# Performance work log

Hardware: AMD Instinct MI355X
Metric: run time of the kernel (lower is better)

Reference implementation:

```python
import jax, jax.numpy as jnp
import numpy as np

# dims: S sets, M max items, DIN input feat, DM model dim (= head_size), H heads, L layers
S, M, DIN, DM, H, DH, L = 48, 128, 128, 128, 4, 128, 2
ALPHA = 0.3  # tf.keras.layers.LeakyReLU default alpha


def gelu(x):
    return jax.nn.gelu(x, approximate=False)  # tf.nn.gelu default is exact


def leaky(x):
    return jnp.where(x >= 0, x, ALPHA * x)


def set_norm(x, size):
    # masked per-set normalization over all items*features; pad rows (feature-sum == 0) are zeroed
    d = x.shape[-1]
    mask = (jnp.sum(x, axis=-1, keepdims=True) != 0).astype(x.dtype)  # [S,M,1]
    denom = size * d  # [S]
    mean = jnp.sum(x, axis=(1, 2)) / denom
    diff = x - mean[:, None, None]
    var = jnp.sum(jnp.square(diff) * mask, axis=(1, 2)) / denom
    return diff / (jnp.sqrt(var)[:, None, None] + 1e-8) * mask


def masked_softmax(s):
    # original masks by *nonzero score values*, not an additive bias
    mask = s != 0
    e = jnp.where(mask, jnp.exp(s - jnp.max(s, axis=-1, keepdims=True)), 0.0)
    return e / (jnp.sum(e, axis=-1, keepdims=True) + 1e-10)


def attention(x, wq, wk, wv, wh):
    split = lambda z: z.reshape(z.shape[0], z.shape[1], H, DH).transpose(0, 2, 1, 3)  # [S,H,M,D]
    q, k, v = split(x @ wq), split(x @ wk), split(x @ wv)
    s = jnp.einsum('shmd,shnd->shmn', q, k) / np.float32(np.sqrt(DH))
    a = masked_softmax(s)
    o = jnp.einsum('shmn,shnd->shmd', a, v).transpose(0, 2, 1, 3).reshape(x.shape[0], x.shape[1], H * DH)
    return o @ wh


def forward(x, size, W_proj, Wq, Wk, Wv, Wh, Wfc, Wc, w2):
    mask = (jnp.sum(x != 0, axis=-1, keepdims=True) > 0).astype(x.dtype)  # [S,M,1] valid-item mask
    h = gelu(x @ W_proj) * mask
    for l in range(L):
        a = attention(h, Wq[l], Wk[l], Wv[l], Wh[l]) * mask
        h = set_norm(h + a, size)
        f = gelu(h @ Wfc[l]) * mask
        h = set_norm(h + f, size)
    # cross_set_score (tuple branch, x == y): pairwise per-head set scores
    z = (h @ Wc).reshape(h.shape[0], h.shape[1], H, DH).transpose(0, 2, 1, 3)  # [S,H,M,D]
    s = leaky(jnp.einsum('jhmd,ihnd->jihmn', z, z) / np.float32(np.sqrt(DH)))  # [Sy,Sx,H,My,Mx]
    scores = jnp.sum(s, axis=(-1, -2)) / size[None, :, None] / np.float32(M)  # [Sy,Sx,H]
    return scores @ w2  # [Sy,Sx,1]


def setup_inputs() -> dict:
    key = jax.random.key(0)
    ks = jax.random.split(key, 10)
    x = jax.random.normal(ks[0], (S, M, DIN), jnp.float32)
    x_size = jax.random.randint(ks[1], (S,), 1, M + 1, jnp.int32)
    x = x * (jnp.arange(M)[None, :] < x_size[:, None])[:, :, None]  # zero-pad beyond set size
    sc = lambda n: np.float32(1.0 / np.sqrt(n))
    W_proj = jax.random.normal(ks[2], (DIN, DM), jnp.float32) * sc(DIN)
    Wq = jax.random.normal(ks[3], (L, DM, H * DH), jnp.float32) * sc(DM)
    Wk = jax.random.normal(ks[4], (L, DM, H * DH), jnp.float32) * sc(DM)
    Wv = jax.random.normal(ks[5], (L, DM, H * DH), jnp.float32) * sc(DM)
    Wh = jax.random.normal(ks[6], (L, H * DH, DM), jnp.float32) * sc(H * DH)
    Wfc = jax.random.normal(ks[7], (L, DM, DM), jnp.float32) * sc(DM)
    Wc = jax.random.normal(ks[8], (DM, H * DH), jnp.float32) * sc(DM)
    w2 = jax.random.normal(ks[9], (H, 1), jnp.float32) * sc(H)
    return dict(x=x, x_size=x_size, W_proj=W_proj, Wq=Wq, Wk=Wk, Wv=Wv, Wh=Wh, Wfc=Wfc, Wc=Wc, w2=w2)


def reference(x, x_size, W_proj, Wq, Wk, Wv, Wh, Wfc, Wc, w2):
    size = jnp.maximum(x_size, 1).astype(jnp.float32)
    return forward(x, size, W_proj, Wq, Wk, Wv, Wh, Wfc, Wc, w2)
```

## Files before the change

kernel.cpp:

```cpp
#include <hip/hip_runtime.h>
#include <hip/hip_bf16.h>
#include <math.h>

typedef unsigned short u16;
typedef short bf16x8 __attribute__((ext_vector_type(8)));
typedef float f32x4 __attribute__((ext_vector_type(4)));
typedef float f32x16 __attribute__((ext_vector_type(16)));

__device__ __forceinline__ u16 f2b(float f){
  union { float f; unsigned u; } c; c.f = f;
  unsigned u = c.u;
  unsigned r = (u + 0x7fffu + ((u >> 16) & 1u)) >> 16;
  return (u16)r;
}
__device__ __forceinline__ unsigned pack2(float a, float b){
  return (unsigned)f2b(a) | ((unsigned)f2b(b) << 16);
}
__device__ __forceinline__ float gelu_f(float x){
  return 0.5f * x * (1.0f + erff(x * 0.70710678118654752f));
}

__global__ __launch_bounds__(256) void prep_weights(
    const float* __restrict__ Wproj, const float* __restrict__ Wq,
    const float* __restrict__ Wk,    const float* __restrict__ Wv,
    const float* __restrict__ Whp,   const float* __restrict__ Wfc,
    const float* __restrict__ Wc,    u16* __restrict__ wT)
{
  __shared__ __align__(16) u16 Ah[128*136];
  __shared__ __align__(16) u16 Bv[128*136];
  int bid = blockIdx.x, tid = threadIdx.x;
  if (bid < 312) {
    int cid = bid * 256 + tid;
    if (cid >= 34816 && cid < 67584) return;
    int region, lh = 0, c;
    if      (cid < 2048)  { region = 0; c = cid; }
    else if (cid < 18432) { int o = cid - 2048;  region = 1; lh = o >> 11; c = o & 2047; }
    else if (cid < 34816) { int o = cid - 18432; region = 2; lh = o >> 11; c = o & 2047; }
    else if (cid < 71680) { int o = cid - 67584; region = 5; lh = o >> 11; c = o & 2047; }
    else                  { int o = cid - 71680; region = 6; lh = o >> 11; c = o & 2047; }
    int l16 = c & 15, quad = (c >> 4) & 3, ks = (c >> 6) & 3, nt = c >> 8;
    int n = nt * 16 + l16, kb = ks * 32 + quad * 8;
    int l = lh >> 2, hh = lh & 3;
    const float rs = 0.08838834764831845f;
    u16 tmp[8];
#pragma unroll
    for (int e = 0; e < 8; ++e) {
      int k = kb + e;
      float v;
      switch (region) {
        case 0: v = Wproj[k * 128 + n]; break;
        case 1: v = Wq[l * 65536 + k * 512 + hh * 128 + n] * rs; break;
        case 2: v = Wk[l * 65536 + k * 512 + hh * 128 + n]; break;
        case 5: v = Wfc[lh * 16384 + k * 128 + n]; break;
        default: v = Wc[k * 512 + lh * 128 + n]; break;
      }
      tmp[e] = f2b(v);
    }
    *(uint4*)(wT + (size_t)cid * 8) = *(uint4*)tmp;
    return;
  }
  int lhb = bid - 312; int l = lhb >> 2, hh = lhb & 3;
#pragma unroll
  for (int it = 0; it < 64; ++it) {
    int idx = it * 256 + tid;
    int a = idx & 127, b = idx >> 7;
    Ah[a * 136 + b] = f2b(Whp[l * 65536 + (hh * 128 + b) * 128 + a]);
    Bv[b * 136 + a] = f2b(Wv[l * 65536 + b * 512 + hh * 128 + a]);
  }
  __syncthreads();
  int wv = tid >> 6, lane = tid & 63, quad = lane >> 4, l16 = lane & 15;
  f32x4 acc[2][8] = {};
  for (int ks = 0; ks < 4; ++ks) {
    bf16x8 aF[2], bF[8];
#pragma unroll
    for (int i = 0; i < 2; ++i)
      aF[i] = *(const bf16x8*)(Ah + ((wv*2+i)*16 + l16)*136 + ks*32 + quad*8);
#pragma unroll
    for (int n = 0; n < 8; ++n)
      bF[n] = *(const bf16x8*)(Bv + (n*16 + l16)*136 + ks*32 + quad*8);
#pragma unroll
    for (int i = 0; i < 2; ++i)
#pragma unroll
      for (int n = 0; n < 8; ++n)
        acc[i][n] = __builtin_amdgcn_mfma_f32_16x16x32_bf16(aF[i], bF[n], acc[i][n], 0, 0, 0);
  }
  size_t base = 278528 + (size_t)lhb * 16384;
#pragma unroll
  for (int i = 0; i < 2; ++i)
#pragma unroll
    for (int n2 = 0; n2 < 8; ++n2)
#pragma unroll
      for (int g = 0; g < 4; ++g) {
        int n = (wv*2+i)*16 + quad*4 + g;
        int k = n2*16 + l16;
        wT[base + (size_t)((((n>>4)*4 + (k>>5))*4 + ((k>>3)&3))*16 + (n&15))*8 + (k&7)]
            = f2b(acc[i][n2][g]);
      }
}

__device__ __forceinline__ void gemm_g8(const u16* A, const u16* __restrict__ Bg,
    f32x4* acc, int wv, int quad, int l16, int lane){
#pragma unroll
  for (int ks = 0; ks < 4; ++ks){
    bf16x8 aF = *(const bf16x8*)(A + (wv*16 + l16)*136 + ks*32 + quad*8);
    bf16x8 bF[8];
#pragma unroll
    for (int n = 0; n < 8; ++n)
      bF[n] = *(const bf16x8*)(Bg + ((size_t)((n*4 + ks)*64 + lane))*8);
#pragma unroll
    for (int n = 0; n < 8; ++n)
      acc[n] = __builtin_amdgcn_mfma_f32_16x16x32_bf16(aF, bF[n], acc[n], 0, 0, 0);
  }
}

__device__ __forceinline__ void write_rm8(u16* dst, f32x4* acc,
                                          int wv, int quad, int l16){
#pragma unroll
  for (int n = 0; n < 8; ++n)
#pragma unroll
    for (int g = 0; g < 4; ++g)
      dst[(wv*16 + quad*4 + g)*136 + n*16 + l16] = f2b(acc[n][g]);
}

__device__ __forceinline__ void write_tr8(u16* dst, f32x4* acc,
                                          int wv, int quad, int l16){
#pragma unroll
  for (int n = 0; n < 8; ++n)
#pragma unroll
    for (int g = 0; g < 4; ++g)
      dst[(n*16 + l16)*136 + wv*16 + quad*4 + g] = f2b(acc[n][g]);
}

__device__ __forceinline__ void block_reduce2(float &s1, float &s2,
                                              float* red, int wv, int lane){
#pragma unroll
  for (int off = 1; off < 64; off <<= 1){
    s1 += __shfl_xor(s1, off, 64);
    s2 += __shfl_xor(s2, off, 64);
  }
  if (lane == 0){ red[wv*2] = s1; red[wv*2+1] = s2; }
  __syncthreads();
  s1 = red[0]+red[2]+red[4]+red[6]+red[8]+red[10]+red[12]+red[14];
  s2 = red[1]+red[3]+red[5]+red[7]+red[9]+red[11]+red[13]+red[15];
  __syncthreads();
}

__global__ __launch_bounds__(512, 2) void trunk(
    const float* __restrict__ x, const int* __restrict__ xsize,
    const u16* __restrict__ wT, u16* __restrict__ zg)
{
  __shared__ __align__(16) u16 hA[128*136];
  __shared__ __align__(16) u16 qP[128*136];
  __shared__ __align__(16) u16 kB[128*136];
  __shared__ __align__(16) u16 vB[128*136];
  __shared__ float svalid[128];
  __shared__ float red[16];
  int tid = threadIdx.x;
  int wv = tid >> 6, lane = tid & 63, quad = lane >> 4, l16 = lane & 15;
  int s = blockIdx.x;
  int sz = xsize[s]; if (sz < 1) sz = 1;
  int Mt = (sz + 15) >> 4, Mk = (sz + 31) >> 5;
  float den = (float)sz * 128.0f;

#pragma unroll
  for (int it = 0; it < 4; ++it) {
    int ch = tid + it * 512; int r = ch >> 4, cc = ch & 15;
    const float* p = x + ((size_t)s * 128 + r) * 128 + cc * 8;
    float4 u0 = *(const float4*)p, u1 = *(const float4*)(p + 4);
    int nz = (u0.x!=0.f)|(u0.y!=0.f)|(u0.z!=0.f)|(u0.w!=0.f)|
             (u1.x!=0.f)|(u1.y!=0.f)|(u1.z!=0.f)|(u1.w!=0.f);
    nz |= __shfl_xor(nz,1,64); nz |= __shfl_xor(nz,2,64);
    nz |= __shfl_xor(nz,4,64); nz |= __shfl_xor(nz,8,64);
    if ((tid & 15) == 0) svalid[r] = nz ? 1.f : 0.f;
    uint4 w;
    w.x = pack2(u0.x,u0.y); w.y = pack2(u0.z,u0.w);
    w.z = pack2(u1.x,u1.y); w.w = pack2(u1.z,u1.w);
    *(uint4*)(hA + r*136 + cc*8) = w;
  }
  __syncthreads();

  f32x4 hR[8];
  {
    f32x4 acc[8] = {};
    gemm_g8(hA, wT, acc, wv, quad, l16, lane);
    __syncthreads();
#pragma unroll
    for (int n2 = 0; n2 < 8; ++n2)
#pragma unroll
      for (int g = 0; g < 4; ++g) {
        int row = wv*16 + quad*4 + g;
        float gg = gelu_f(acc[n2][g]) * svalid[row];
        hR[n2][g] = gg;
        hA[row*136 + n2*16 + l16] = f2b(gg);
      }
    __syncthreads();
  }

  for (int l = 0; l < 2; ++l) {
    f32x4 aR[8] = {};
    for (int hh = 0; hh < 4; ++hh) {
      int lh = l * 4 + hh;
      {
        f32x4 qa[8] = {};
        gemm_g8(hA, wT + 16384 + lh*16384, qa, wv, quad, l16, lane);
        write_rm8(qP, qa, wv, quad, l16);
      }
      {
        f32x4 ka[8] = {};
        gemm_g8(hA, wT + 147456 + lh*16384, ka, wv, quad, l16, lane);
        write_rm8(kB, ka, wv, quad, l16);
      }
      {
        f32x4 va[8] = {};
        gemm_g8(hA, wT + 278528 + lh*16384, va, wv, quad, l16, lane);
        write_tr8(vB, va, wv, quad, l16);
      }
      __syncthreads();
      bool act = wv < Mt;
      bf16x8 qA[4];
#pragma unroll
      for (int ks = 0; ks < 4; ++ks)
        qA[ks] = *(const bf16x8*)(qP + (wv*16 + l16)*136 + ks*32 + quad*8);
      if (act) {
        f32x4 sacc[8] = {};
#pragma unroll
        for (int ks = 0; ks < 4; ++ks) {
          bf16x8 bF[8];
#pragma unroll
          for (int j = 0; j < 8; ++j)
            if (j < Mt) bF[j] = *(const bf16x8*)(kB + (j*16+l16)*136 + ks*32 + quad*8);
#pragma unroll
          for (int j = 0; j < 8; ++j)
            if (j < Mt) sacc[j] = __builtin_amdgcn_mfma_f32_16x16x32_bf16(qA[ks], bF[j], sacc[j], 0, 0, 0);
        }
        for (int g = 0; g < 4; ++g) {
          float vals[8]; float rmax = -1e30f;
#pragma unroll
          for (int j = 0; j < 8; ++j)
            if (j < Mt) {
              float v = sacc[j][g];
              vals[j] = v;
              rmax = fmaxf(rmax, v);
            }
          for (int off = 1; off < 16; off <<= 1) rmax = fmaxf(rmax, __shfl_xor(rmax, off, 64));
          if (sz < 128) rmax = fmaxf(rmax, 0.0f);
          float rsum = 0.f;
#pragma unroll
          for (int j = 0; j < 8; ++j)
            if (j < Mt) {
              float e = (vals[j] != 0.0f) ? expf(vals[j] - rmax) : 0.0f;
              vals[j] = e; rsum += e;
            }
          for (int off = 1; off < 16; off <<= 1) rsum += __shfl_xor(rsum, off, 64);
          float inv = 1.0f / (rsum + 1e-10f);
#pragma unroll
          for (int j = 0; j < 8; ++j)
            if (j < Mt) sacc[j][g] = vals[j] * inv;
        }
#pragma unroll
        for (int j = 0; j < 8; ++j)
          if (j < Mt)
#pragma unroll
            for (int g = 0; g < 4; ++g)
              qP[(wv*16 + quad*4 + g)*136 + j*16 + l16] = f2b(sacc[j][g]);
        for (int ks = 0; ks < Mk; ++ks) {
          bf16x8 aF = *(const bf16x8*)(qP + (wv*16 + l16)*136 + ks*32 + quad*8);
          bf16x8 bF[8];
#pragma unroll
          for (int n = 0; n < 8; ++n)
            bF[n] = *(const bf16x8*)(vB + (n*16+l16)*136 + ks*32 + quad*8);
#pragma unroll
          for (int n = 0; n < 8; ++n)
            aR[n] = __builtin_amdgcn_mfma_f32_16x16x32_bf16(aF, bF[n], aR[n], 0, 0, 0);
        }
      }
      __syncthreads();
    }

    {
      float ls1 = 0.f, ls2 = 0.f;
#pragma unroll
      for (int n2 = 0; n2 < 8; ++n2)
#pragma unroll
        for (int g = 0; g < 4; ++g) {
          int row = wv*16 + quad*4 + g;
          float u = hR[n2][g] + aR[n2][g] * svalid[row];
          hR[n2][g] = u;
          ls1 += u; ls2 += u * u;
        }
      block_reduce2(ls1, ls2, red, wv, lane);
      float mean = ls1 / den;
      float var = ls2 / den - mean * mean; if (var < 0.f) var = 0.f;
      float inv = 1.0f / (sqrtf(var) + 1e-8f);
#pragma unroll
      for (int n2 = 0; n2 < 8; ++n2)
#pragma unroll
        for (int g = 0; g < 4; ++g) {
          int row = wv*16 + quad*4 + g;
          float hn = (hR[n2][g] - mean) * inv * svalid[row];
          hR[n2][g] = hn;
          hA[row*136 + n2*16 + l16] = f2b(hn);
        }
      __syncthreads();
    }
    {
      f32x4 fa[8] = {};
      gemm_g8(hA, wT + 540672 + l*16384, fa, wv, quad, l16, lane);
      float ls1 = 0.f, ls2 = 0.f;
#pragma unroll
      for (int n2 = 0; n2 < 8; ++n2)
#pragma unroll
        for (int g = 0; g < 4; ++g) {
          int row = wv*16 + quad*4 + g;
          float u = hR[n2][g] + gelu_f(fa[n2][g]) * svalid[row];
          hR[n2][g] = u;
          ls1 += u; ls2 += u * u;
        }
      block_reduce2(ls1, ls2, red, wv, lane);
      float mean = ls1 / den;
      float var = ls2 / den - mean * mean; if (var < 0.f) var = 0.f;
      float inv = 1.0f / (sqrtf(var) + 1e-8f);
#pragma unroll
      for (int n2 = 0; n2 < 8; ++n2)
#pragma unroll
        for (int g = 0; g < 4; ++g) {
          int row = wv*16 + quad*4 + g;
          float hn = (hR[n2][g] - mean) * inv * svalid[row];
          hR[n2][g] = hn;
          hA[row*136 + n2*16 + l16] = f2b(hn);
        }
      __syncthreads();
    }
  }

  for (int hh = 0; hh < 4; ++hh) {
    f32x4 za[8] = {};
    gemm_g8(hA, wT + 573440 + hh*16384, za, wv, quad, l16, lane);
#pragma unroll
    for (int n2 = 0; n2 < 8; ++n2)
#pragma unroll
      for (int g = 0; g < 4; ++g) {
        int row = wv*16 + quad*4 + g;
        int col = n2*16 + l16;
        zg[((size_t)(s*4 + hh)*128 + row)*128 + col] = f2b(za[n2][g]);
      }
  }
}

__global__ __launch_bounds__(256) void cross_kernel(
    const u16* __restrict__ zg, float* __restrict__ Tbuf, const int* __restrict__ xsize)
{
  __shared__ __align__(16) u16 bufA[16384];
  __shared__ __align__(16) u16 bufB[16384];
  __shared__ float red[4];
  int tid = threadIdx.x, wave = tid >> 6, lane = tid & 63;
  int t4 = blockIdx.x;
  int pr = t4 >> 2, hh = t4 & 3;
  float jf = (97.0f - sqrtf(9409.0f - 8.0f * (float)pr)) * 0.5f;
  int j = (int)jf; if (j > 47) j = 47; if (j < 0) j = 0;
  while (j > 0 && j * 48 - (j * (j - 1)) / 2 > pr) --j;
  while ((j + 1) * 48 - ((j + 1) * j) / 2 <= pr) ++j;
  int i = j + pr - (j * 48 - (j * (j - 1)) / 2);
  int sj = xsize[j]; if (sj < 1) sj = 1;
  int si = xsize[i]; if (si < 1) si = 1;
  int MjT = (sj + 31) >> 5, MiT = (si + 31) >> 5;
  size_t basej = ((size_t)j * 4 + hh) << 14;
  size_t basei = ((size_t)i * 4 + hh) << 14;
#pragma unroll
  for (int t = 0; t < 8; ++t) {
    int c = t * 256 + tid;
    int m = c & 31, half = (c >> 5) & 1, ks = (c >> 6) & 7, g = c >> 9;
    int row = g * 32 + m, col = ks * 16 + half * 8;
    if (g < MjT) *(uint4*)(bufA + c * 8) = *(const uint4*)(zg + basej + row * 128 + col);
    if (g < MiT) *(uint4*)(bufB + c * 8) = *(const uint4*)(zg + basei + row * 128 + col);
  }
  __syncthreads();
  int gA = (wave >> 1) * 2, gB = (wave & 1) * 2;
  bool a0 = gA < MjT, a1 = (gA + 1) < MjT;
  bool b0 = gB < MiT, b1 = (gB + 1) < MiT;
  f32x16 acc[2][2] = {};
  if ((a0 || a1) && (b0 || b1)) {
    for (int ks = 0; ks < 8; ++ks) {
      bf16x8 aF[2], bF[2];
      if (a0) aF[0] = *(const bf16x8*)(bufA + ((gA    ) * 8 + ks) * 512 + lane * 8);
      if (a1) aF[1] = *(const bf16x8*)(bufA + ((gA + 1) * 8 + ks) * 512 + lane * 8);
      if (b0) bF[0] = *(const bf16x8*)(bufB + ((gB    ) * 8 + ks) * 512 + lane * 8);
      if (b1) bF[1] = *(const bf16x8*)(bufB + ((gB + 1) * 8 + ks) * 512 + lane * 8);
      if (a0 && b0) acc[0][0] = __builtin_amdgcn_mfma_f32_32x32x16_bf16(aF[0], bF[0], acc[0][0], 0, 0, 0);
      if (a0 && b1) acc[0][1] = __builtin_amdgcn_mfma_f32_32x32x16_bf16(aF[0], bF[1], acc[0][1], 0, 0, 0);
      if (a1 && b0) acc[1][0] = __builtin_amdgcn_mfma_f32_32x32x16_bf16(aF[1], bF[0], acc[1][0], 0, 0, 0);
      if (a1 && b1) acc[1][1] = __builtin_amdgcn_mfma_f32_32x32x16_bf16(aF[1], bF[1], acc[1][1], 0, 0, 0);
    }
  }
  float s1 = 0.f, s2 = 0.f;
#pragma unroll
  for (int ii = 0; ii < 2; ++ii)
#pragma unroll
    for (int jj = 0; jj < 2; ++jj) {
      bool tact = (ii ? a1 : a0) && (jj ? b1 : b0);
      if (tact)
#pragma unroll
        for (int r = 0; r < 16; ++r) {
          float a = acc[ii][jj][r];
          s1 += a; s2 += fabsf(a);
        }
    }
  const float rs = 0.08838834764831845f;
  float tp = rs * (0.65f * s1 + 0.35f * s2);
  for (int off = 1; off < 64; off <<= 1) tp += __shfl_xor(tp, off, 64);
  if (lane == 0) red[wave] = tp;
  __syncthreads();
  if (tid == 0)
    Tbuf[((j * 48 + i) << 2) + hh] = red[0] + red[1] + red[2] + red[3];
}

__global__ __launch_bounds__(256) void final_kernel(
    const float* __restrict__ Tbuf, const float* __restrict__ w2,
    const int* __restrict__ xsize, float* __restrict__ out)
{
  int idx = blockIdx.x * 256 + threadIdx.x;
  if (idx >= 2304) return;
  int a = idx / 48, b = idx - a * 48;
  int j = a < b ? a : b, i = a < b ? b : a;
  float t = 0.f;
  for (int h = 0; h < 4; ++h) t += Tbuf[((j * 48 + i) << 2) + h] * w2[h];
  int szb = xsize[b]; if (szb < 1) szb = 1;
  out[idx] = t / ((float)szb * 128.0f);
}

extern "C" void kernel_launch(void* const* d_in, const int* in_sizes, int n_in,
                              void* d_out, int out_size, void* d_ws, size_t ws_size,
                              hipStream_t stream)
{
  const float* x     = (const float*)d_in[0];
  const int*   xsize = (const int*)d_in[1];
  const float* Wproj = (const float*)d_in[2];
  const float* Wq    = (const float*)d_in[3];
  const float* Wk    = (const float*)d_in[4];
  const float* Wv    = (const float*)d_in[5];
  const float* Whp   = (const float*)d_in[6];
  const float* Wfc   = (const float*)d_in[7];
  const float* Wc    = (const float*)d_in[8];
  const float* w2    = (const float*)d_in[9];
  float* out = (float*)d_out;

  char* ws = (char*)d_ws;
  size_t off = 0;
  auto alloc = [&](size_t bytes) -> char* {
    char* p = ws + off;
    off += (bytes + 255) & ~(size_t)255;
    return p;
  };
  u16*   wT   = (u16*)  alloc(638976 * 2);
  float* Tbuf = (float*)alloc(9216 * 4);
  u16*   zg   = (u16*)  alloc((size_t)3145728 * 2);

  prep_weights<<<320, 256, 0, stream>>>(Wproj, Wq, Wk, Wv, Whp, Wfc, Wc, wT);
  trunk<<<48, 512, 0, stream>>>(x, xsize, wT, zg);
  cross_kernel<<<4704, 256, 0, stream>>>(zg, Tbuf, xsize);
  final_kernel<<<9, 256, 0, stream>>>(Tbuf, w2, xsize, out);
}
```

Baseline: 269.3 us.

## Split trunk GEMMs across 16 waves with 1024-thread blocks

The per-set trunk kernel now launches 1024 threads (16 waves) instead of 512. Each wave computes a 16-row by 64-column half-tile of every projection GEMM rather than a full 16x128 strip, halving per-wave accumulator registers. Only 48 blocks run on a many-CU GPU, so the aim is more in-flight waves per block on the serial trunk. The softmax stage still uses the first 8 waves, so an extra barrier is added between softmax and the PV product. Upper waves idle during softmax, and the extra barriers add sync cost.

Measured after the change: 283.5 us. 1.05x slower.

```diff
diff --git a/kernel.cpp b/kernel.cpp
--- a/kernel.cpp
+++ b/kernel.cpp
@@ -98,37 +98,37 @@
       }
 }
 
-__device__ __forceinline__ void gemm_g8(const u16* A, const u16* __restrict__ Bg,
-    f32x4* acc, int wv, int quad, int l16, int lane){
+__device__ __forceinline__ void gemm_g4(const u16* A, const u16* __restrict__ Bg,
+    f32x4* acc, int mt, int nh, int quad, int l16, int lane){
 #pragma unroll
   for (int ks = 0; ks < 4; ++ks){
-    bf16x8 aF = *(const bf16x8*)(A + (wv*16 + l16)*136 + ks*32 + quad*8);
-    bf16x8 bF[8];
-#pragma unroll
-    for (int n = 0; n < 8; ++n)
-      bF[n] = *(const bf16x8*)(Bg + ((size_t)((n*4 + ks)*64 + lane))*8);
-#pragma unroll
-    for (int n = 0; n < 8; ++n)
+    bf16x8 aF = *(const bf16x8*)(A + (mt*16 + l16)*136 + ks*32 + quad*8);
+    bf16x8 bF[4];
+#pragma unroll
+    for (int n = 0; n < 4; ++n)
+      bF[n] = *(const bf16x8*)(Bg + ((size_t)(((nh*4+n)*4 + ks)*64 + lane))*8);
+#pragma unroll
+    for (int n = 0; n < 4; ++n)
       acc[n] = __builtin_amdgcn_mfma_f32_16x16x32_bf16(aF, bF[n], acc[n], 0, 0, 0);
   }
 }
 
-__device__ __forceinline__ void write_rm8(u16* dst, f32x4* acc,
-                                          int wv, int quad, int l16){
-#pragma unroll
-  for (int n = 0; n < 8; ++n)
+__device__ __forceinline__ void write_rm4(u16* dst, f32x4* acc,
+                                          int mt, int nh, int quad, int l16){
+#pragma unroll
+  for (int n = 0; n < 4; ++n)
 #pragma unroll
     for (int g = 0; g < 4; ++g)
-      dst[(wv*16 + quad*4 + g)*136 + n*16 + l16] = f2b(acc[n][g]);
-}
-
-__device__ __forceinline__ void write_tr8(u16* dst, f32x4* acc,
-                                          int wv, int quad, int l16){
-#pragma unroll
-  for (int n = 0; n < 8; ++n)
+      dst[(mt*16 + quad*4 + g)*136 + (nh*4+n)*16 + l16] = f2b(acc[n][g]);
+}
+
+__device__ __forceinline__ void write_tr4(u16* dst, f32x4* acc,
+                                          int mt, int nh, int quad, int l16){
+#pragma unroll
+  for (int n = 0; n < 4; ++n)
 #pragma unroll
     for (int g = 0; g < 4; ++g)
-      dst[(n*16 + l16)*136 + wv*16 + quad*4 + g] = f2b(acc[n][g]);
+      dst[((nh*4+n)*16 + l16)*136 + mt*16 + quad*4 + g] = f2b(acc[n][g]);
 }
 
 __device__ __forceinline__ void block_reduce2(float &s1, float &s2,
@@ -140,12 +140,13 @@
   }
   if (lane == 0){ red[wv*2] = s1; red[wv*2+1] = s2; }
   __syncthreads();
-  s1 = red[0]+red[2]+red[4]+red[6]+red[8]+red[10]+red[12]+red[14];
-  s2 = red[1]+red[3]+red[5]+red[7]+red[9]+red[11]+red[13]+red[15];
-  __syncthreads();
-}
-
-__global__ __launch_bounds__(512, 2) void trunk(
+  s1 = 0.f; s2 = 0.f;
+#pragma unroll
+  for (int w = 0; w < 16; ++w){ s1 += red[w*2]; s2 += red[w*2+1]; }
+  __syncthreads();
+}
+
+__global__ __launch_bounds__(1024, 1) void trunk(
     const float* __restrict__ x, const int* __restrict__ xsize,
     const u16* __restrict__ wT, u16* __restrict__ zg)
 {
@@ -154,17 +155,18 @@
   __shared__ __align__(16) u16 kB[128*136];
   __shared__ __align__(16) u16 vB[128*136];
   __shared__ float svalid[128];
-  __shared__ float red[16];
+  __shared__ float red[32];
   int tid = threadIdx.x;
   int wv = tid >> 6, lane = tid & 63, quad = lane >> 4, l16 = lane & 15;
+  int mt = wv >> 1, nh = wv & 1;
   int s = blockIdx.x;
   int sz = xsize[s]; if (sz < 1) sz = 1;
   int Mt = (sz + 15) >> 4, Mk = (sz + 31) >> 5;
   float den = (float)sz * 128.0f;
 
 #pragma unroll
-  for (int it = 0; it < 4; ++it) {
-    int ch = tid + it * 512; int r = ch >> 4, cc = ch & 15;
+  for (int it = 0; it < 2; ++it) {
+    int ch = tid + it * 1024; int r = ch >> 4, cc = ch & 15;
     const float* p = x + ((size_t)s * 128 + r) * 128 + cc * 8;
     float4 u0 = *(const float4*)p, u1 = *(const float4*)(p + 4);
     int nz = (u0.x!=0.f)|(u0.y!=0.f)|(u0.z!=0.f)|(u0.w!=0.f)|
@@ -179,49 +181,49 @@
   }
   __syncthreads();
 
-  f32x4 hR[8];
+  f32x4 hR[4];
   {
-    f32x4 acc[8] = {};
-    gemm_g8(hA, wT, acc, wv, quad, l16, lane);
+    f32x4 acc[4] = {};
+    gemm_g4(hA, wT, acc, mt, nh, quad, l16, lane);
     __syncthreads();
 #pragma unroll
-    for (int n2 = 0; n2 < 8; ++n2)
+    for (int n2 = 0; n2 < 4; ++n2)
 #pragma unroll
       for (int g = 0; g < 4; ++g) {
-        int row = wv*16 + quad*4 + g;
+        int row = mt*16 + quad*4 + g;
         float gg = gelu_f(acc[n2][g]) * svalid[row];
         hR[n2][g] = gg;
-        hA[row*136 + n2*16 + l16] = f2b(gg);
+        hA[row*136 + (nh*4+n2)*16 + l16] = f2b(gg);
       }
     __syncthreads();
   }
 
   for (int l = 0; l < 2; ++l) {
-    f32x4 aR[8] = {};
+    f32x4 aR[4] = {};
     for (int hh = 0; hh < 4; ++hh) {
       int lh = l * 4 + hh;
+      __syncthreads();
       {
-        f32x4 qa[8] = {};
-        gemm_g8(hA, wT + 16384 + lh*16384, qa, wv, quad, l16, lane);
-        write_rm8(qP, qa, wv, quad, l16);
+        f32x4 qa[4] = {};
+        gemm_g4(hA, wT + 16384 + lh*16384, qa, mt, nh, quad, l16, lane);
+        write_rm4(qP, qa, mt, nh, quad, l16);
       }
       {
-        f32x4 ka[8] = {};
-        gemm_g8(hA, wT + 147456 + lh*16384, ka, wv, quad, l16, lane);
-        write_rm8(kB, ka, wv, quad, l16);
+        f32x4 ka[4] = {};
+        gemm_g4(hA, wT + 147456 + lh*16384, ka, mt, nh, quad, l16, lane);
+        write_rm4(kB, ka, mt, nh, quad, l16);
       }
       {
-        f32x4 va[8] = {};
-        gemm_g8(hA, wT + 278528 + lh*16384, va, wv, quad, l16, lane);
-        write_tr8(vB, va, wv, quad, l16);
+        f32x4 va[4] = {};
+        gemm_g4(hA, wT + 278528 + lh*16384, va, mt, nh, quad, l16, lane);
+        write_tr4(vB, va, mt, nh, quad, l16);
       }
       __syncthreads();
-      bool act = wv < Mt;
-      bf16x8 qA[4];
-#pragma unroll
-      for (int ks = 0; ks < 4; ++ks)
-        qA[ks] = *(const bf16x8*)(qP + (wv*16 + l16)*136 + ks*32 + quad*8);
-      if (act) {
+      if (wv < 8 && wv < Mt) {
+        bf16x8 qA[4];
+#pragma unroll
+        for (int ks = 0; ks < 4; ++ks)
+          qA[ks] = *(const bf16x8*)(qP + (wv*16 + l16)*136 + ks*32 + quad*8);
         f32x4 sacc[8] = {};
 #pragma unroll
         for (int ks = 0; ks < 4; ++ks) {
@@ -263,27 +265,29 @@
 #pragma unroll
             for (int g = 0; g < 4; ++g)
               qP[(wv*16 + quad*4 + g)*136 + j*16 + l16] = f2b(sacc[j][g]);
+      }
+      __syncthreads();
+      if (mt < Mt) {
         for (int ks = 0; ks < Mk; ++ks) {
-          bf16x8 aF = *(const bf16x8*)(qP + (wv*16 + l16)*136 + ks*32 + quad*8);
-          bf16x8 bF[8];
-#pragma unroll
-          for (int n = 0; n < 8; ++n)
-            bF[n] = *(const bf16x8*)(vB + (n*16+l16)*136 + ks*32 + quad*8);
-#pragma unroll
-          for (int n = 0; n < 8; ++n)
+          bf16x8 aF = *(const bf16x8*)(qP + (mt*16 + l16)*136 + ks*32 + quad*8);
+          bf16x8 bF[4];
+#pragma unroll
+          for (int n = 0; n < 4; ++n)
+            bF[n] = *(const bf16x8*)(vB + ((nh*4+n)*16+l16)*136 + ks*32 + quad*8);
+#pragma unroll
+          for (int n = 0; n < 4; ++n)
             aR[n] = __builtin_amdgcn_mfma_f32_16x16x32_bf16(aF, bF[n], aR[n], 0, 0, 0);
         }
       }
-      __syncthreads();
     }
 
     {
       float ls1 = 0.f, ls2 = 0.f;
 #pragma unroll
-      for (int n2 = 0; n2 < 8; ++n2)
+      for (int n2 = 0; n2 < 4; ++n2)
 #pragma unroll
         for (int g = 0; g < 4; ++g) {
-          int row = wv*16 + quad*4 + g;
+          int row = mt*16 + quad*4 + g;
           float u = hR[n2][g] + aR[n2][g] * svalid[row];
           hR[n2][g] = u;
           ls1 += u; ls2 += u * u;
@@ -293,25 +297,25 @@
       float var = ls2 / den - mean * mean; if (var < 0.f) var = 0.f;
       float inv = 1.0f / (sqrtf(var) + 1e-8f);
 #pragma unroll
-      for (int n2 = 0; n2 < 8; ++n2)
+      for (int n2 = 0; n2 < 4; ++n2)
 #pragma unroll
         for (int g = 0; g < 4; ++g) {
-          int row = wv*16 + quad*4 + g;
+          int row = mt*16 + quad*4 + g;
           float hn = (hR[n2][g] - mean) * inv * svalid[row];
           hR[n2][g] = hn;
-          hA[row*136 + n2*16 + l16] = f2b(hn);
+          hA[row*136 + (nh*4+n2)*16 + l16] = f2b(hn);
         }
       __syncthreads();
     }
     {
-      f32x4 fa[8] = {};
-      gemm_g8(hA, wT + 540672 + l*16384, fa, wv, quad, l16, lane);
+      f32x4 fa[4] = {};
+      gemm_g4(hA, wT + 540672 + l*16384, fa, mt, nh, quad, l16, lane);
       float ls1 = 0.f, ls2 = 0.f;
 #pragma unroll
-      for (int n2 = 0; n2 < 8; ++n2)
+      for (int n2 = 0; n2 < 4; ++n2)
 #pragma unroll
         for (int g = 0; g < 4; ++g) {
-          int row = wv*16 + quad*4 + g;
+          int row = mt*16 + quad*4 + g;
           float u = hR[n2][g] + gelu_f(fa[n2][g]) * svalid[row];
           hR[n2][g] = u;
           ls1 += u; ls2 += u * u;
@@ -321,27 +325,27 @@
       float var = ls2 / den - mean * mean; if (var < 0.f) var = 0.f;
       float inv = 1.0f / (sqrtf(var) + 1e-8f);
 #pragma unroll
-      for (int n2 = 0; n2 < 8; ++n2)
+      for (int n2 = 0; n2 < 4; ++n2)
 #pragma unroll
         for (int g = 0; g < 4; ++g) {
-          int row = wv*16 + quad*4 + g;
+          int row = mt*16 + quad*4 + g;
           float hn = (hR[n2][g] - mean) * inv * svalid[row];
           hR[n2][g] = hn;
-          hA[row*136 + n2*16 + l16] = f2b(hn);
+          hA[row*136 + (nh*4+n2)*16 + l16] = f2b(hn);
         }
       __syncthreads();
     }
   }
 
   for (int hh = 0; hh < 4; ++hh) {
-    f32x4 za[8] = {};
-    gemm_g8(hA, wT + 573440 + hh*16384, za, wv, quad, l16, lane);
-#pragma unroll
-    for (int n2 = 0; n2 < 8; ++n2)
+    f32x4 za[4] = {};
+    gemm_g4(hA, wT + 573440 + hh*16384, za, mt, nh, quad, l16, lane);
+#pragma unroll
+    for (int n2 = 0; n2 < 4; ++n2)
 #pragma unroll
       for (int g = 0; g < 4; ++g) {
-        int row = wv*16 + quad*4 + g;
-        int col = n2*16 + l16;
+        int row = mt*16 + quad*4 + g;
+        int col = (nh*4+n2)*16 + l16;
         zg[((size_t)(s*4 + hh)*128 + row)*128 + col] = f2b(za[n2][g]);
       }
   }
@@ -456,7 +460,7 @@
   u16*   zg   = (u16*)  alloc((size_t)3145728 * 2);
 
   prep_weights<<<320, 256, 0, stream>>>(Wproj, Wq, Wk, Wv, Whp, Wfc, Wc, wT);
-  trunk<<<48, 512, 0, stream>>>(x, xsize, wT, zg);
+  trunk<<<48, 1024, 0, stream>>>(x, xsize, wT, zg);
   cross_kernel<<<4704, 256, 0, stream>>>(zg, Tbuf, xsize);
   final_kernel<<<9, 256, 0, stream>>>(Tbuf, w2, xsize, out);
 }
```
